# Optimization experiments

Measured on AMD Instinct MI355X. Metric: run time of the kernel, lower is better.

The kernel has to match this reference:

```python
import jax, jax.numpy as jnp
import numpy as np

LAMDA = 0.5

def setup_inputs() -> dict:
    key = jax.random.key(0)
    k1, k2 = jax.random.split(key)
    X_set = jax.random.normal(k1, (8192, 128), dtype=jnp.float32)
    Y_set = jax.random.randint(k2, (8192,), 0, 100, dtype=jnp.int64)
    return {"X_set": X_set, "Y_set": Y_set}

def _pairwise_euclidean(X):
    # X: [N, D] -> D: [N, N] euclidean distances (torch.cdist p=2)
    sq_norms = jnp.sum(X * X, axis=1)  # [N]
    sq = sq_norms[:, None] + sq_norms[None, :] - 2.0 * (X @ X.T)  # [N, N]
    sq = jnp.maximum(sq, 0.0)
    # safe sqrt (zero diagonal) to stay grad-safe under jit
    pos = sq > 0.0
    return jnp.where(pos, jnp.sqrt(jnp.where(pos, sq, 1.0)), 0.0)

def reference(X_set, Y_set):
    X = X_set.reshape(X_set.shape[0], -1)
    D = _pairwise_euclidean(X)  # [N, N]
    same = Y_set[:, None] == Y_set[None, :]  # [N, N] bool
    # Class loop in original == sum of within-class distances (incl. zero diag)
    # minus lamda * sum over all ordered cross-class pairs (each unordered
    # cross pair is counted once for each of its two classes -> full mask).
    pos_sum = jnp.sum(jnp.where(same, D, 0.0))
    neg_sum = jnp.sum(jnp.where(same, 0.0, D))
    return pos_sum - LAMDA * neg_sum
```

## Files before the change

### kernel.cpp

```cpp
#include <hip/hip_runtime.h>

#define N_ROWS 8192
#define DIM    128
#define BM     128
#define NBLK   (N_ROWS / BM)
#define NTRI   (NBLK * (NBLK + 1) / 2)

#define BLOB_PER_RB 65536
#define BLOB_PER_PH 16384

typedef _Float16 half8 __attribute__((ext_vector_type(8)));
typedef float    f32x16 __attribute__((ext_vector_type(16)));

__global__ __launch_bounds__(256)
void prep_tiled(const float* __restrict__ X, char* __restrict__ blob,
                float* __restrict__ norms, double* __restrict__ gsum,
                unsigned int* __restrict__ counter)
{
    const int t    = blockIdx.x * 256 + threadIdx.x;
    const int kq   = t & 15;
    const int p    = kq >> 2;
    const int ksub = kq & 3;
    const int row  = t >> 4;

    if (t == 0) { *gsum = 0.0; *counter = 0u; }

    const float4* src = (const float4*)(X + (size_t)row * DIM + p * 32 + ksub * 8);
    const float4 v0 = src[0], v1 = src[1];
    const float xs[8] = {v0.x, v0.y, v0.z, v0.w, v1.x, v1.y, v1.z, v1.w};

    half8 h, l;
    float ns = 0.0f;
    #pragma unroll
    for (int i = 0; i < 8; ++i) {
        const float x = xs[i];
        const _Float16 hh = (_Float16)x;
        h[i] = hh;
        l[i] = (_Float16)(x - (float)hh);
        ns = fmaf(x, x, ns);
    }

    const int rb   = row >> 7;
    const int r    = row & 127;
    const int g32  = (r >> 5) & 3;
    const int q    = ksub >> 1;
    const int slot = (r & 31) + (ksub & 1) * 32;
    char* base = blob + (size_t)rb * BLOB_PER_RB + p * BLOB_PER_PH
               + g32 * 4096 + q * 1024 + slot * 16;
    *(half8*)(base)        = h;
    *(half8*)(base + 2048) = l;

    #pragma unroll
    for (int off = 1; off <= 8; off <<= 1) ns += __shfl_xor(ns, off);
    if ((t & 15) == 0) norms[row] = ns;
}

__global__ __launch_bounds__(256, 4)
void pairsum_mfma(const char* __restrict__ blob, const float* __restrict__ norms,
                  const int* __restrict__ Y, double* __restrict__ gsum,
                  unsigned int* __restrict__ counter, float* __restrict__ out)
{
    const int kb = blockIdx.x;
    int bi = (int)((129.0f - sqrtf(fmaf(-8.0f, (float)kb, 129.0f * 129.0f))) * 0.5f);
    while ((bi + 1) * (129 - (bi + 1)) / 2 <= kb) ++bi;
    while (bi * (129 - bi) / 2 > kb) --bi;
    const int bj = bi + (kb - bi * (129 - bi) / 2);
    const int i0 = bi * BM, j0 = bj * BM;

    const int tid  = threadIdx.x;
    const int lane = tid & 63;
    const int w    = tid >> 6;
    const int wy   = w >> 1;
    const int wx   = w & 1;
    const int lr   = lane & 31;
    const int lh   = lane >> 5;

    __shared__ float nI[BM], nJ[BM];
    __shared__ int   yI[BM], yJ[BM];
    __shared__ double wsum[4];

    if (tid < BM) { nI[tid] = norms[i0 + tid]; yI[tid] = Y[i0 + tid]; }
    else { const int r = tid & (BM - 1); nJ[r] = norms[j0 + r]; yJ[r] = Y[j0 + r]; }
    __syncthreads();

    const char* Apan = blob + (size_t)bi * BLOB_PER_RB;
    const char* Bpan = blob + (size_t)bj * BLOB_PER_RB;

    f32x16 acc[2][2];
    #pragma unroll
    for (int m = 0; m < 2; ++m)
        #pragma unroll
        for (int n = 0; n < 2; ++n)
            #pragma unroll
            for (int r = 0; r < 16; ++r)
                acc[m][n][r] = 0.0f;

    #pragma unroll
    for (int p = 0; p < 4; ++p) {
        #pragma unroll
        for (int q = 0; q < 2; ++q) {
            half8 ah[2], al[2], bh[2], bl[2];
            #pragma unroll
            for (int m = 0; m < 2; ++m) {
                const char* a = Apan + p * BLOB_PER_PH + (wy * 2 + m) * 4096
                              + q * 1024 + lane * 16;
                ah[m] = *(const half8*)a;
                al[m] = *(const half8*)(a + 2048);
                const char* b = Bpan + p * BLOB_PER_PH + (wx * 2 + m) * 4096
                              + q * 1024 + lane * 16;
                bh[m] = *(const half8*)b;
                bl[m] = *(const half8*)(b + 2048);
            }
            #pragma unroll
            for (int m = 0; m < 2; ++m)
                #pragma unroll
                for (int n = 0; n < 2; ++n) {
                    acc[m][n] = __builtin_amdgcn_mfma_f32_32x32x16_f16(ah[m], bh[n], acc[m][n], 0, 0, 0);
                    acc[m][n] = __builtin_amdgcn_mfma_f32_32x32x16_f16(ah[m], bl[n], acc[m][n], 0, 0, 0);
                    acc[m][n] = __builtin_amdgcn_mfma_f32_32x32x16_f16(al[m], bh[n], acc[m][n], 0, 0, 0);
                }
        }
    }

    float s = 0.0f;
    float nJv[2]; int yJv[2];
    #pragma unroll
    for (int n = 0; n < 2; ++n) {
        const int lj = wx * 64 + n * 32 + lr;
        nJv[n] = nJ[lj]; yJv[n] = yJ[lj];
    }
    #pragma unroll
    for (int m = 0; m < 2; ++m) {
        #pragma unroll
        for (int r = 0; r < 16; ++r) {
            const int rowin = (r & 3) + 8 * (r >> 2) + 4 * lh;
            const int li = wy * 64 + m * 32 + rowin;
            const float ni = nI[li];
            const int   yi = yI[li];
            const int   gi = i0 + li;
            #pragma unroll
            for (int n = 0; n < 2; ++n) {
                const int gj = j0 + wx * 64 + n * 32 + lr;
                float sq = fmaf(-2.0f, acc[m][n][r], ni + nJv[n]);
                sq = fmaxf(sq, 0.0f);
                const float d = __builtin_amdgcn_sqrtf(sq);
                if (gi < gj) s = fmaf((yi == yJv[n]) ? 1.0f : -0.5f, d, s);
            }
        }
    }

    #pragma unroll
    for (int off = 32; off > 0; off >>= 1) s += __shfl_down(s, off);
    if (lane == 0) wsum[w] = (double)s;
    __syncthreads();
    if (tid == 0) {
        atomicAdd(gsum, wsum[0] + wsum[1] + wsum[2] + wsum[3]);
        __threadfence();
        const unsigned int old = atomicAdd(counter, 1u);
        if (old == NTRI - 1) {
            __threadfence();
            const double tot = atomicAdd(gsum, 0.0);
            out[0] = (float)(2.0 * tot);
        }
    }
}

__global__ void finalize_kernel(const double* __restrict__ gsum, float* __restrict__ out)
{
    out[0] = (float)(2.0 * gsum[0]);
}

#define LDSPAD 4
#define LDB (BM + LDSPAD)
__global__ __launch_bounds__(256)
void pairsum_valu(const float* __restrict__ X, const int* __restrict__ Y,
                  double* __restrict__ gsum)
{
    const int bj = blockIdx.x, bi = blockIdx.y;
    if (bi > bj) return;
    const int tid = threadIdx.x;
    const int i0 = bi * BM, j0 = bj * BM;
    __shared__ float As[32][LDB], Bs[32][LDB];
    __shared__ float nI[BM], nJ[BM];
    __shared__ int yI[BM], yJ[BM];
    __shared__ double wsum[4];
    {
        const int r = tid & (BM - 1);
        const bool isJ = tid >= BM;
        const int row = (isJ ? j0 : i0) + r;
        const float4* p = (const float4*)(X + (size_t)row * DIM);
        float s = 0.f;
        #pragma unroll
        for (int q = 0; q < DIM / 4; ++q) {
            float4 v = p[q];
            s = fmaf(v.x, v.x, s); s = fmaf(v.y, v.y, s);
            s = fmaf(v.z, v.z, s); s = fmaf(v.w, v.w, s);
        }
        if (isJ) { nJ[r] = s; yJ[r] = Y[row]; }
        else     { nI[r] = s; yI[r] = Y[row]; }
    }
    float dot[8][8];
    #pragma unroll
    for (int m = 0; m < 8; ++m)
        #pragma unroll
        for (int n = 0; n < 8; ++n) dot[m][n] = 0.f;
    const int tx = tid & 15, ty = tid >> 4;
    for (int kc = 0; kc < DIM; kc += 32) {
        __syncthreads();
        #pragma unroll
        for (int p = 0; p < 4; ++p) {
            const int s2 = p * 256 + tid;
            const int row = s2 >> 3, kg = s2 & 7;
            const float4 va = *(const float4*)(X + (size_t)(i0 + row) * DIM + kc + kg * 4);
            const float4 vb = *(const float4*)(X + (size_t)(j0 + row) * DIM + kc + kg * 4);
            As[kg*4+0][row] = va.x; As[kg*4+1][row] = va.y;
            As[kg*4+2][row] = va.z; As[kg*4+3][row] = va.w;
            Bs[kg*4+0][row] = vb.x; Bs[kg*4+1][row] = vb.y;
            Bs[kg*4+2][row] = vb.z; Bs[kg*4+3][row] = vb.w;
        }
        __syncthreads();
        #pragma unroll
        for (int k = 0; k < 32; ++k) {
            float a[8], b[8];
            *(float4*)&a[0] = *(const float4*)&As[k][ty*8];
            *(float4*)&a[4] = *(const float4*)&As[k][ty*8+4];
            *(float4*)&b[0] = *(const float4*)&Bs[k][tx*8];
            *(float4*)&b[4] = *(const float4*)&Bs[k][tx*8+4];
            #pragma unroll
            for (int m = 0; m < 8; ++m)
                #pragma unroll
                for (int n = 0; n < 8; ++n)
                    dot[m][n] = fmaf(a[m], b[n], dot[m][n]);
        }
    }
    float s = 0.f;
    const int ib = ty * 8, jb = tx * 8;
    #pragma unroll
    for (int m = 0; m < 8; ++m) {
        const int gi = i0 + ib + m;
        const float ni = nI[ib + m];
        const int yi = yI[ib + m];
        #pragma unroll
        for (int n = 0; n < 8; ++n) {
            const int gj = j0 + jb + n;
            float sq = fmaf(-2.f, dot[m][n], ni + nJ[jb + n]);
            sq = fmaxf(sq, 0.f);
            const float d = __builtin_amdgcn_sqrtf(sq);
            if (gi < gj) s = fmaf((yi == yJ[jb + n]) ? 1.0f : -0.5f, d, s);
        }
    }
    #pragma unroll
    for (int off = 32; off > 0; off >>= 1) s += __shfl_down(s, off);
    const int lane = tid & 63, wid = tid >> 6;
    if (lane == 0) wsum[wid] = (double)s;
    __syncthreads();
    if (tid == 0) atomicAdd(gsum, wsum[0] + wsum[1] + wsum[2] + wsum[3]);
}

extern "C" void kernel_launch(void* const* d_in, const int* in_sizes, int n_in,
                              void* d_out, int out_size, void* d_ws, size_t ws_size,
                              hipStream_t stream)
{
    const float* X = (const float*)d_in[0];
    const int*   Y = (const int*)d_in[1];
    float* out = (float*)d_out;

    const size_t OFF_BLOB = 64;
    const size_t OFF_NORM = OFF_BLOB + (size_t)NBLK * BLOB_PER_RB;
    const size_t REQ      = OFF_NORM + (size_t)N_ROWS * 4;

    double*       gsum    = (double*)d_ws;
    unsigned int* counter = (unsigned int*)((char*)d_ws + 8);

    if (ws_size >= REQ) {
        char*  blob  = (char*)d_ws + OFF_BLOB;
        float* norms = (float*)((char*)d_ws + OFF_NORM);
        prep_tiled<<<(N_ROWS * 16) / 256, 256, 0, stream>>>(X, blob, norms, gsum, counter);
        pairsum_mfma<<<NTRI, 256, 0, stream>>>(blob, norms, Y, gsum, counter, out);
    } else {
        hipMemsetAsync(d_ws, 0, sizeof(double), stream);
        dim3 grid(NBLK, NBLK);
        pairsum_valu<<<grid, 256, 0, stream>>>(X, Y, gsum);
        finalize_kernel<<<1, 1, 0, stream>>>(gsum, out);
    }
}
```

Measured before the change: 131.7 us.

## Stage MFMA operand panels through LDS with async global_load_lds double buffering

Replaces the direct global-to-register loads of A/B half panels with async global_load_lds copies into a 64 KB LDS double buffer. The next K-phase is prefetched while MFMAs run on the current one, with explicit vmcnt waits, barriers and raised wave priority around the MFMA block. Norm and label loads move to registers early and are written to LDS after the main loop. The 64 KB LDS footprint forces occupancy down, so launch bounds drop from 4 to 2 blocks per CU, trading latency hiding from occupancy for explicit prefetching.

```diff
diff --git a/kernel.cpp b/kernel.cpp
--- a/kernel.cpp
+++ b/kernel.cpp
@@ -11,6 +11,15 @@
 
 typedef _Float16 half8 __attribute__((ext_vector_type(8)));
 typedef float    f32x16 __attribute__((ext_vector_type(16)));
+
+typedef const __attribute__((address_space(1))) unsigned int glb_uint;
+typedef __attribute__((address_space(3))) unsigned int lds_uint;
+
+__device__ inline void gload_lds16(const void* g, void* l)
+{
+    __builtin_amdgcn_global_load_lds((glb_uint*)(uintptr_t)g,
+                                     (lds_uint*)(uintptr_t)l, 16, 0, 0);
+}
 
 __global__ __launch_bounds__(256)
 void prep_tiled(const float* __restrict__ X, char* __restrict__ blob,
@@ -55,7 +64,7 @@
     if ((t & 15) == 0) norms[row] = ns;
 }
 
-__global__ __launch_bounds__(256, 4)
+__global__ __launch_bounds__(256, 2)
 void pairsum_mfma(const char* __restrict__ blob, const float* __restrict__ norms,
                   const int* __restrict__ Y, double* __restrict__ gsum,
                   unsigned int* __restrict__ counter, float* __restrict__ out)
@@ -75,17 +84,29 @@
     const int lr   = lane & 31;
     const int lh   = lane >> 5;
 
+    const bool isJ = tid >= BM;
+    const int  nr  = tid & (BM - 1);
+    const float myNorm = norms[(isJ ? j0 : i0) + nr];
+    const int   myY    = Y[(isJ ? j0 : i0) + nr];
+
+    __shared__ __align__(16) char tile[65536];
     __shared__ float nI[BM], nJ[BM];
     __shared__ int   yI[BM], yJ[BM];
     __shared__ double wsum[4];
 
-    if (tid < BM) { nI[tid] = norms[i0 + tid]; yI[tid] = Y[i0 + tid]; }
-    else { const int r = tid & (BM - 1); nJ[r] = norms[j0 + r]; yJ[r] = Y[j0 + r]; }
-    __syncthreads();
-
     const char* Apan = blob + (size_t)bi * BLOB_PER_RB;
     const char* Bpan = blob + (size_t)bj * BLOB_PER_RB;
 
+    auto STAGE = [&](int p, int s) {
+        #pragma unroll
+        for (int r = 0; r < 4; ++r) {
+            gload_lds16(Apan + p * BLOB_PER_PH + r * 4096 + tid * 16,
+                        tile + s * 32768 + r * 4096 + tid * 16);
+            gload_lds16(Bpan + p * BLOB_PER_PH + r * 4096 + tid * 16,
+                        tile + s * 32768 + 16384 + r * 4096 + tid * 16);
+        }
+    };
+
     f32x16 acc[2][2];
     #pragma unroll
     for (int m = 0; m < 2; ++m)
@@ -95,32 +116,50 @@
             for (int r = 0; r < 16; ++r)
                 acc[m][n][r] = 0.0f;
 
+    STAGE(0, 0);
+    STAGE(1, 1);
+
     #pragma unroll
     for (int p = 0; p < 4; ++p) {
-        #pragma unroll
-        for (int q = 0; q < 2; ++q) {
-            half8 ah[2], al[2], bh[2], bl[2];
+        if (p < 3) asm volatile("s_waitcnt vmcnt(8)" ::: "memory");
+        else       asm volatile("s_waitcnt vmcnt(0)" ::: "memory");
+        __builtin_amdgcn_s_barrier();
+        __builtin_amdgcn_sched_barrier(0);
+
+        const char* Ab = tile + (p & 1) * 32768;
+        const char* Bb = Ab + 16384;
+        half8 ah[2][2], al[2][2], bh[2][2], bl[2][2];
+        #pragma unroll
+        for (int q = 0; q < 2; ++q)
             #pragma unroll
             for (int m = 0; m < 2; ++m) {
-                const char* a = Apan + p * BLOB_PER_PH + (wy * 2 + m) * 4096
-                              + q * 1024 + lane * 16;
-                ah[m] = *(const half8*)a;
-                al[m] = *(const half8*)(a + 2048);
-                const char* b = Bpan + p * BLOB_PER_PH + (wx * 2 + m) * 4096
-                              + q * 1024 + lane * 16;
-                bh[m] = *(const half8*)b;
-                bl[m] = *(const half8*)(b + 2048);
+                const int ga = (wy * 2 + m) * 4096 + q * 1024 + lane * 16;
+                ah[q][m] = *(const half8*)(Ab + ga);
+                al[q][m] = *(const half8*)(Ab + ga + 2048);
+                const int gb = (wx * 2 + m) * 4096 + q * 1024 + lane * 16;
+                bh[q][m] = *(const half8*)(Bb + gb);
+                bl[q][m] = *(const half8*)(Bb + gb + 2048);
             }
+        __builtin_amdgcn_s_setprio(1);
+        #pragma unroll
+        for (int q = 0; q < 2; ++q)
             #pragma unroll
             for (int m = 0; m < 2; ++m)
                 #pragma unroll
                 for (int n = 0; n < 2; ++n) {
-                    acc[m][n] = __builtin_amdgcn_mfma_f32_32x32x16_f16(ah[m], bh[n], acc[m][n], 0, 0, 0);
-                    acc[m][n] = __builtin_amdgcn_mfma_f32_32x32x16_f16(ah[m], bl[n], acc[m][n], 0, 0, 0);
-                    acc[m][n] = __builtin_amdgcn_mfma_f32_32x32x16_f16(al[m], bh[n], acc[m][n], 0, 0, 0);
+                    acc[m][n] = __builtin_amdgcn_mfma_f32_32x32x16_f16(ah[q][m], bh[q][n], acc[m][n], 0, 0, 0);
+                    acc[m][n] = __builtin_amdgcn_mfma_f32_32x32x16_f16(ah[q][m], bl[q][n], acc[m][n], 0, 0, 0);
+                    acc[m][n] = __builtin_amdgcn_mfma_f32_32x32x16_f16(al[q][m], bh[q][n], acc[m][n], 0, 0, 0);
                 }
-        }
-    }
+        __builtin_amdgcn_s_setprio(0);
+        __builtin_amdgcn_sched_barrier(0);
+        __builtin_amdgcn_s_barrier();
+        if (p + 2 < 4) STAGE(p + 2, p & 1);
+    }
+
+    if (isJ) { nJ[nr] = myNorm; yJ[nr] = myY; }
+    else     { nI[nr] = myNorm; yI[nr] = myY; }
+    __syncthreads();
 
     float s = 0.0f;
     float nJv[2]; int yJv[2];
```

Result: no change. 130.0 us (-1.3%).
